# Kernel tuning notes

Hardware: AMD Instinct MI355X
Metric: run time of the kernel (lower is better)

## Reference

```python
import jax, jax.numpy as jnp
import numpy as np

K = 4  # cross2d scan directions


def _selective_scan(u, delta, A, Bs, Cs, Ds, delta_bias):
    # u, delta: (B, K*D, L); A: (K*D, N); Bs, Cs: (B, K, N, L); Ds: (K*D,)
    Bsz, KD, L = u.shape
    D = KD // K
    N = A.shape[1]
    delta = jax.nn.softplus(delta + delta_bias[None, :, None])
    u4 = u.reshape(Bsz, K, D, L)
    dl = delta.reshape(Bsz, K, D, L)
    A4 = A.reshape(K, D, N)

    def step(h, inp):
        dl_t, u_t, B_t, C_t = inp  # (B,K,D),(B,K,D),(B,K,N),(B,K,N)
        dA = jnp.exp(dl_t[..., None] * A4)                     # (B,K,D,N)
        h = dA * h + (dl_t * u_t)[..., None] * B_t[:, :, None, :]
        y = jnp.einsum('bkdn,bkn->bkd', h, C_t)
        return h, y

    h0 = jnp.zeros((Bsz, K, D, N), u.dtype)
    inps = (jnp.moveaxis(dl, -1, 0), jnp.moveaxis(u4, -1, 0),
            jnp.moveaxis(Bs, -1, 0), jnp.moveaxis(Cs, -1, 0))
    _, ys = jax.lax.scan(step, h0, inps)                       # (L,B,K,D)
    ys = jnp.moveaxis(ys, 0, -1)                               # (B,K,D,L)
    return ys + Ds.reshape(1, K, D, 1) * u4


def setup_inputs() -> dict:
    key = jax.random.key(0)
    ks = jax.random.split(key, 12)
    B, H, W, d_model = 8, 48, 48, 96
    d_inner, N, R = 192, 16, 6
    s = 0.05
    return {
        'x': jax.random.normal(ks[0], (B, H, W, d_model), jnp.float32),
        'in_proj_w': jax.random.normal(ks[1], (2 * d_inner, d_model), jnp.float32) * s,
        'conv_w': jax.random.normal(ks[2], (d_inner, 1, 3, 3), jnp.float32) * s,
        'conv_b': jax.random.normal(ks[3], (d_inner,), jnp.float32) * s,
        'x_proj_w': jax.random.normal(ks[4], (K, R + 2 * N, d_inner), jnp.float32) * s,
        'dt_projs_w': jax.random.normal(ks[5], (K, d_inner, R), jnp.float32) * s,
        'dt_projs_b': jax.random.normal(ks[6], (K, d_inner), jnp.float32) * s,
        'A_logs': jax.random.uniform(ks[7], (K * d_inner, N), jnp.float32),
        'Ds': jax.random.normal(ks[8], (K * d_inner,), jnp.float32) * s,
        'ln_g': jnp.ones((d_inner,), jnp.float32),
        'ln_b': jnp.zeros((d_inner,), jnp.float32),
        'out_proj_w': jax.random.normal(ks[9], (d_model, d_inner), jnp.float32) * s,
    }


def reference(x, in_proj_w, conv_w, conv_b, x_proj_w, dt_projs_w, dt_projs_b,
              A_logs, Ds, ln_g, ln_b, out_proj_w):
    B, H, W, _ = x.shape
    Din = dt_projs_w.shape[1]
    N = A_logs.shape[1]
    R = dt_projs_w.shape[2]
    L = H * W

    # in_proj + gate split (channel-last)
    xz = x @ in_proj_w.T                                    # (B,H,W,2*Din)
    xc, z = jnp.split(xz, 2, axis=-1)
    z = jax.nn.silu(z)

    # depthwise conv (NCHW) + SiLU
    xc = jnp.transpose(xc, (0, 3, 1, 2))                    # (B,Din,H,W)
    xc = jax.lax.conv_general_dilated(
        xc, conv_w, (1, 1), 'SAME', feature_group_count=Din,
        dimension_numbers=('NCHW', 'OIHW', 'NCHW')) + conv_b[None, :, None, None]
    xc = jax.nn.silu(xc)

    # cross-scan (cross2d): row-major, col-major, and their reverses
    x0 = xc.reshape(B, Din, L)
    x1 = jnp.transpose(xc, (0, 1, 3, 2)).reshape(B, Din, L)
    xs = jnp.stack([x0, x1, x0[..., ::-1], x1[..., ::-1]], axis=1)  # (B,K,Din,L)

    # grouped projections
    x_dbl = jnp.einsum('bkdl,kcd->bkcl', xs, x_proj_w)
    dts, Bm, Cm = jnp.split(x_dbl, [R, R + N], axis=2)      # (B,K,R,L),(B,K,N,L),(B,K,N,L)
    dts = jnp.einsum('bkrl,kdr->bkdl', dts, dt_projs_w)

    A = -jnp.exp(A_logs.astype(jnp.float32))                # (K*Din, N)
    ys = _selective_scan(xs.reshape(B, K * Din, L), dts.reshape(B, K * Din, L),
                         A, Bm, Cm, Ds.astype(jnp.float32),
                         dt_projs_b.reshape(-1).astype(jnp.float32))  # (B,K,Din,L)

    # cross-merge (inverse of cross-scan)
    y02 = ys[:, 0] + ys[:, 2, :, ::-1]
    y13 = ys[:, 1] + ys[:, 3, :, ::-1]
    y = y02 + jnp.transpose(y13.reshape(B, Din, W, H), (0, 1, 3, 2)).reshape(B, Din, L)
    y = jnp.transpose(y.reshape(B, Din, H, W), (0, 2, 3, 1))  # (B,H,W,Din)

    # LayerNorm over channels
    mu = y.mean(-1, keepdims=True)
    var = y.var(-1, keepdims=True)
    y = (y - mu) / jnp.sqrt(var + 1e-5) * ln_g + ln_b

    y = y * z
    return y @ out_proj_w.T
```

## Files before the change

kernel.cpp:

```cpp
#include <hip/hip_runtime.h>
#include <math.h>

#define HD   48
#define WD   48
#define BB   8
#define DM   96
#define DIN  192
#define LL   2304
#define NN   16
#define RR   6
#define KK   4
#define CH   32
#define NC   72

#define LOG2E 1.44269504f
#define LN2   0.69314718f

__global__ __launch_bounds__(256) void k_inproj(const float* __restrict__ x,
                                                const float* __restrict__ w,
                                                float* __restrict__ xc,
                                                float* __restrict__ zb) {
    __shared__ float sa[64 * 97];
    __shared__ float sb[96 * 68];
    const int tid = threadIdx.x;
    const int p0 = blockIdx.x * 64;
    const int n0 = blockIdx.y * 64;

    for (int i = tid; i < 64 * 96; i += 256) {
        int r = i / 96, c = i % 96;
        sa[r * 97 + c] = x[(size_t)(p0 + r) * 96 + c];
    }
    for (int i = tid; i < 64 * 96; i += 256) {
        int n = i / 96, c = i % 96;
        sb[c * 68 + n] = w[(size_t)(n0 + n) * 96 + c];
    }
    __syncthreads();

    const int tx = tid & 15, ty = tid >> 4;
    const int r0 = ty * 4, c0 = tx * 4;
    float acc[4][4] = {};
    for (int k = 0; k < 96; ++k) {
        float a0 = sa[(r0 + 0) * 97 + k];
        float a1 = sa[(r0 + 1) * 97 + k];
        float a2 = sa[(r0 + 2) * 97 + k];
        float a3 = sa[(r0 + 3) * 97 + k];
        float4 bv = *(const float4*)&sb[k * 68 + c0];
        acc[0][0] += a0 * bv.x; acc[0][1] += a0 * bv.y; acc[0][2] += a0 * bv.z; acc[0][3] += a0 * bv.w;
        acc[1][0] += a1 * bv.x; acc[1][1] += a1 * bv.y; acc[1][2] += a1 * bv.z; acc[1][3] += a1 * bv.w;
        acc[2][0] += a2 * bv.x; acc[2][1] += a2 * bv.y; acc[2][2] += a2 * bv.z; acc[2][3] += a2 * bv.w;
        acc[3][0] += a3 * bv.x; acc[3][1] += a3 * bv.y; acc[3][2] += a3 * bv.z; acc[3][3] += a3 * bv.w;
    }
    for (int i = 0; i < 4; ++i) {
        int p = p0 + r0 + i;
        for (int j = 0; j < 4; ++j) {
            int n = n0 + c0 + j;
            float v = acc[i][j];
            if (n < DIN) {
                xc[(size_t)p * DIN + n] = v;
            } else {
                float s = v / (1.f + __expf(-v));
                zb[(size_t)p * DIN + (n - DIN)] = s;
            }
        }
    }
}

__global__ __launch_bounds__(192) void k_conv(const float* __restrict__ xc,
                                              const float* __restrict__ cw,
                                              const float* __restrict__ cb,
                                              float* __restrict__ xs0,
                                              float* __restrict__ xs1) {
    const int p = blockIdx.x;
    const int d = threadIdx.x;
    const int b = p / LL;
    const int hw = p % LL;
    const int h = hw / WD, w = hw % WD;

    float acc = cb[d];
    #pragma unroll
    for (int ky = 0; ky < 3; ++ky) {
        int hy = h + ky - 1;
        if ((unsigned)hy >= HD) continue;
        #pragma unroll
        for (int kx = 0; kx < 3; ++kx) {
            int wx = w + kx - 1;
            if ((unsigned)wx >= WD) continue;
            acc += xc[((size_t)(b * HD + hy) * WD + wx) * DIN + d] * cw[d * 9 + ky * 3 + kx];
        }
    }
    float v = acc / (1.f + __expf(-acc));
    xs0[((size_t)b * LL + h * WD + w) * DIN + d] = v;
    xs1[((size_t)b * LL + w * HD + h) * DIN + d] = v;
}

__global__ __launch_bounds__(256) void k_xproj(const float* __restrict__ xs0,
                                               const float* __restrict__ xs1,
                                               const float* __restrict__ wxp,
                                               float* __restrict__ dtr,
                                               float* __restrict__ Bt,
                                               float* __restrict__ Ct) {
    __shared__ float sxs[64 * 196];
    __shared__ float sw[40 * 192];
    const int k = blockIdx.y;
    const int b = blockIdx.z;
    const int tid = threadIdx.x;
    const int t0 = blockIdx.x * 64;
    const float* src = (k & 1) ? xs1 : xs0;

    for (int i = tid; i < 40 * 48; i += 256) {
        int row = i / 48, j = i % 48;
        float4 v = (row < 38)
            ? ((const float4*)&wxp[((size_t)k * 38 + row) * 192])[j]
            : make_float4(0.f, 0.f, 0.f, 0.f);
        ((float4*)&sw[row * 192])[j] = v;
    }
    for (int i = tid; i < 64 * 48; i += 256) {
        int r = i / 48, j = i % 48;
        int t = t0 + r;
        int ts = (k < 2) ? t : (LL - 1 - t);
        ((float4*)&sxs[r * 196])[j] =
            ((const float4*)&src[((size_t)b * LL + ts) * DIN])[j];
    }
    __syncthreads();

    const int lp = tid & 31;
    const int c0 = (tid >> 5) * 5;
    float acc[2][5] = {};
    const float* x0 = &sxs[lp * 196];
    const float* x1 = &sxs[(lp + 32) * 196];
    for (int d = 0; d < 192; d += 4) {
        float4 a0 = *(const float4*)&x0[d];
        float4 a1 = *(const float4*)&x1[d];
        #pragma unroll
        for (int j = 0; j < 5; ++j) {
            float4 wv = *(const float4*)&sw[(c0 + j) * 192 + d];
            acc[0][j] += a0.x * wv.x + a0.y * wv.y + a0.z * wv.z + a0.w * wv.w;
            acc[1][j] += a1.x * wv.x + a1.y * wv.y + a1.z * wv.z + a1.w * wv.w;
        }
    }

    #pragma unroll
    for (int pp = 0; pp < 2; ++pp) {
        size_t base = (size_t)(b * KK + k) * LL + (t0 + lp + pp * 32);
        #pragma unroll
        for (int j = 0; j < 5; ++j) {
            int c = c0 + j;
            float v = acc[pp][j];
            if (c < RR)               dtr[base * RR + c] = v;
            else if (c < RR + NN)     Bt[base * NN + (c - RR)] = v;
            else if (c < RR + 2 * NN) Ct[base * NN + (c - RR - NN)] = v;
        }
    }
}

__global__ __launch_bounds__(192) void k_scan1(const float* __restrict__ xs0,
                                               const float* __restrict__ xs1,
                                               const float* __restrict__ dtr,
                                               const float* __restrict__ Bt,
                                               const float* __restrict__ A_logs,
                                               const float* __restrict__ dtw,
                                               const float* __restrict__ dtb,
                                               float* __restrict__ hend,
                                               float* __restrict__ ssp) {
    __shared__ __align__(16) float sB[CH * NN];
    __shared__ __align__(16) float sdt[CH * RR];
    const int c = blockIdx.x, k = blockIdx.y, b = blockIdx.z;
    const int d = threadIdx.x;
    const int kd = k * DIN + d;
    const size_t baseBK = (size_t)(b * KK + k) * LL;
    const int t0 = c * CH;

    for (int i = threadIdx.x; i < CH * NN; i += 192) sB[i] = Bt[(baseBK + t0) * NN + i];
    for (int i = threadIdx.x; i < CH * RR; i += 192) sdt[i] = dtr[(baseBK + t0) * RR + i];
    __syncthreads();

    float a2_[NN];
    #pragma unroll
    for (int n = 0; n < NN; ++n) a2_[n] = -__expf(A_logs[(size_t)kd * NN + n]) * LOG2E;
    float w_[RR];
    #pragma unroll
    for (int r = 0; r < RR; ++r) w_[r] = dtw[(size_t)kd * RR + r];
    const float bias = dtb[kd];
    float h[NN];
    #pragma unroll
    for (int n = 0; n < NN; ++n) h[n] = 0.f;
    float sum_sp = 0.f;

    const float* u_src = (k & 1) ? xs1 : xs0;
    float u_next = u_src[((size_t)b * LL + ((k < 2) ? t0 : (LL - 1 - t0))) * DIN + d];

    for (int tt = 0; tt < CH; ++tt) {
        float u = u_next;
        if (tt + 1 < CH) {
            int tn = t0 + tt + 1;
            int ts = (k < 2) ? tn : (LL - 1 - tn);
            u_next = u_src[((size_t)b * LL + ts) * DIN + d];
        }
        const float2* dr = (const float2*)&sdt[tt * RR];
        float2 d0 = dr[0], d1 = dr[1], d2 = dr[2];
        float xv = bias + d0.x * w_[0] + d0.y * w_[1] + d1.x * w_[2]
                        + d1.y * w_[3] + d2.x * w_[4] + d2.y * w_[5];
        float sp = (xv > 15.f) ? xv
                 : __builtin_amdgcn_logf(1.f + __builtin_amdgcn_exp2f(xv * LOG2E)) * LN2;
        sum_sp += sp;
        float du = sp * u;
        const float4* Bp = (const float4*)&sB[tt * NN];
        #pragma unroll
        for (int q = 0; q < 4; ++q) {
            float4 Bv = Bp[q];
            h[4*q+0] = __builtin_amdgcn_exp2f(sp * a2_[4*q+0]) * h[4*q+0] + du * Bv.x;
            h[4*q+1] = __builtin_amdgcn_exp2f(sp * a2_[4*q+1]) * h[4*q+1] + du * Bv.y;
            h[4*q+2] = __builtin_amdgcn_exp2f(sp * a2_[4*q+2]) * h[4*q+2] + du * Bv.z;
            h[4*q+3] = __builtin_amdgcn_exp2f(sp * a2_[4*q+3]) * h[4*q+3] + du * Bv.w;
        }
    }

    size_t ob = (((size_t)(b * KK + k) * NC + c) * DIN + d) * NN;
    #pragma unroll
    for (int q = 0; q < 4; ++q) {
        *(float4*)&hend[ob + 4 * q] = make_float4(h[4*q], h[4*q+1], h[4*q+2], h[4*q+3]);
    }
    ssp[((size_t)c * (BB * KK) + (b * KK + k)) * DIN + d] = sum_sp;
}

__global__ __launch_bounds__(256) void k_comb(float* __restrict__ hend,
                                              const float* __restrict__ ssp,
                                              const float* __restrict__ A_logs) {
    const int gid = blockIdx.x * 256 + threadIdx.x;
    const int n = gid & 15;
    const int dkb = gid >> 4;
    const int d = dkb % DIN;
    const int bk = dkb / DIN;
    const int k = bk & 3;
    const float a2 = -__expf(A_logs[(size_t)(k * DIN + d) * NN + n]) * LOG2E;
    float h = 0.f;
    for (int c = 0; c < NC; ++c) {
        size_t idx = (((size_t)bk * NC + c) * DIN + d) * NN + n;
        float e = hend[idx];
        hend[idx] = h;
        float P = __builtin_amdgcn_exp2f(a2 * ssp[((size_t)c * (BB * KK) + bk) * DIN + d]);
        h = P * h + e;
    }
}

__global__ __launch_bounds__(192) void k_scan2(const float* __restrict__ xs0,
                                               const float* __restrict__ xs1,
                                               const float* __restrict__ dtr,
                                               const float* __restrict__ Bt,
                                               const float* __restrict__ Ct,
                                               const float* __restrict__ A_logs,
                                               const float* __restrict__ Ds,
                                               const float* __restrict__ dtw,
                                               const float* __restrict__ dtb,
                                               const float* __restrict__ hstart,
                                               float* __restrict__ yacc) {
    __shared__ __align__(16) float sB[CH * NN];
    __shared__ __align__(16) float sC[CH * NN];
    __shared__ __align__(16) float sdt[CH * RR];
    const int c = blockIdx.x, k = blockIdx.y, b = blockIdx.z;
    const int d = threadIdx.x;
    const int kd = k * DIN + d;
    const size_t baseBK = (size_t)(b * KK + k) * LL;
    const int t0 = c * CH;

    for (int i = threadIdx.x; i < CH * NN; i += 192) {
        sB[i] = Bt[(baseBK + t0) * NN + i];
        sC[i] = Ct[(baseBK + t0) * NN + i];
    }
    for (int i = threadIdx.x; i < CH * RR; i += 192) sdt[i] = dtr[(baseBK + t0) * RR + i];
    __syncthreads();

    float a2_[NN];
    #pragma unroll
    for (int n = 0; n < NN; ++n) a2_[n] = -__expf(A_logs[(size_t)kd * NN + n]) * LOG2E;
    float w_[RR];
    #pragma unroll
    for (int r = 0; r < RR; ++r) w_[r] = dtw[(size_t)kd * RR + r];
    const float bias = dtb[kd];
    const float Dv = Ds[kd];

    float h[NN];
    size_t hb = (((size_t)(b * KK + k) * NC + c) * DIN + d) * NN;
    #pragma unroll
    for (int q = 0; q < 4; ++q) {
        float4 hv = *(const float4*)&hstart[hb + 4 * q];
        h[4*q] = hv.x; h[4*q+1] = hv.y; h[4*q+2] = hv.z; h[4*q+3] = hv.w;
    }

    const float* u_src = (k & 1) ? xs1 : xs0;
    float u_next = u_src[((size_t)b * LL + ((k < 2) ? t0 : (LL - 1 - t0))) * DIN + d];

    for (int tt = 0; tt < CH; ++tt) {
        float u = u_next;
        if (tt + 1 < CH) {
            int tn = t0 + tt + 1;
            int ts = (k < 2) ? tn : (LL - 1 - tn);
            u_next = u_src[((size_t)b * LL + ts) * DIN + d];
        }
        const float2* dr = (const float2*)&sdt[tt * RR];
        float2 d0 = dr[0], d1 = dr[1], d2 = dr[2];
        float xv = bias + d0.x * w_[0] + d0.y * w_[1] + d1.x * w_[2]
                        + d1.y * w_[3] + d2.x * w_[4] + d2.y * w_[5];
        float sp = (xv > 15.f) ? xv
                 : __builtin_amdgcn_logf(1.f + __builtin_amdgcn_exp2f(xv * LOG2E)) * LN2;
        float du = sp * u;
        const float4* Bp = (const float4*)&sB[tt * NN];
        const float4* Cp = (const float4*)&sC[tt * NN];
        float y = 0.f;
        #pragma unroll
        for (int q = 0; q < 4; ++q) {
            float4 Bv = Bp[q], Cv = Cp[q];
            h[4*q+0] = __builtin_amdgcn_exp2f(sp * a2_[4*q+0]) * h[4*q+0] + du * Bv.x; y += h[4*q+0] * Cv.x;
            h[4*q+1] = __builtin_amdgcn_exp2f(sp * a2_[4*q+1]) * h[4*q+1] + du * Bv.y; y += h[4*q+1] * Cv.y;
            h[4*q+2] = __builtin_amdgcn_exp2f(sp * a2_[4*q+2]) * h[4*q+2] + du * Bv.z; y += h[4*q+2] * Cv.z;
            h[4*q+3] = __builtin_amdgcn_exp2f(sp * a2_[4*q+3]) * h[4*q+3] + du * Bv.w; y += h[4*q+3] * Cv.w;
        }
        y += Dv * u;

        int t = t0 + tt;
        int pos;
        if (k == 0)      pos = t;
        else if (k == 2) pos = LL - 1 - t;
        else if (k == 1) pos = (t % HD) * WD + (t / HD);
        else { int t1 = LL - 1 - t; pos = (t1 % HD) * WD + (t1 / HD); }

        atomicAdd(&yacc[((size_t)b * LL + pos) * DIN + d], y);
    }
}

__global__ __launch_bounds__(256) void k_final(const float* __restrict__ yacc,
                                               const float* __restrict__ zb,
                                               const float* __restrict__ g,
                                               const float* __restrict__ bta,
                                               const float* __restrict__ wo,
                                               float* __restrict__ out) {
    __shared__ float syn[32 * 194];
    __shared__ float swo[96 * 98];
    const int tid = threadIdx.x;
    const int P0 = blockIdx.x * 32;

    {
        const int p = tid >> 3;
        const int q = tid & 7;
        const float* yr = &yacc[((size_t)(P0 + p)) * DIN + q * 24];
        float4 v0 = ((const float4*)yr)[0];
        float4 v1 = ((const float4*)yr)[1];
        float4 v2 = ((const float4*)yr)[2];
        float4 v3 = ((const float4*)yr)[3];
        float4 v4 = ((const float4*)yr)[4];
        float4 v5 = ((const float4*)yr)[5];
        float s  = v0.x+v0.y+v0.z+v0.w + v1.x+v1.y+v1.z+v1.w + v2.x+v2.y+v2.z+v2.w
                 + v3.x+v3.y+v3.z+v3.w + v4.x+v4.y+v4.z+v4.w + v5.x+v5.y+v5.z+v5.w;
        float sq = v0.x*v0.x+v0.y*v0.y+v0.z*v0.z+v0.w*v0.w
                 + v1.x*v1.x+v1.y*v1.y+v1.z*v1.z+v1.w*v1.w
                 + v2.x*v2.x+v2.y*v2.y+v2.z*v2.z+v2.w*v2.w
                 + v3.x*v3.x+v3.y*v3.y+v3.z*v3.z+v3.w*v3.w
                 + v4.x*v4.x+v4.y*v4.y+v4.z*v4.z+v4.w*v4.w
                 + v5.x*v5.x+v5.y*v5.y+v5.z*v5.z+v5.w*v5.w;
        #pragma unroll
        for (int off = 1; off < 8; off <<= 1) {
            s  += __shfl_xor(s, off);
            sq += __shfl_xor(sq, off);
        }
        float mu = s * (1.f / DIN);
        float rs = rsqrtf(sq * (1.f / DIN) - mu * mu + 1e-5f);

        const float* zr = &zb[((size_t)(P0 + p)) * DIN + q * 24];
        const float* gr = &g[q * 24];
        const float* br = &bta[q * 24];
        float* sy = &syn[p * 194 + q * 24];
        #pragma unroll
        for (int j = 0; j < 6; ++j) {
            float4 vv = (j == 0) ? v0 : (j == 1) ? v1 : (j == 2) ? v2
                      : (j == 3) ? v3 : (j == 4) ? v4 : v5;
            float4 gv = ((const float4*)gr)[j];
            float4 bv = ((const float4*)br)[j];
            float4 zv = ((const float4*)zr)[j];
            float t0 = ((vv.x - mu) * rs * gv.x + bv.x) * zv.x;
            float t1 = ((vv.y - mu) * rs * gv.y + bv.y) * zv.y;
            float t2 = ((vv.z - mu) * rs * gv.z + bv.z) * zv.z;
            float t3 = ((vv.w - mu) * rs * gv.w + bv.w) * zv.w;
            ((float2*)sy)[2 * j]     = make_float2(t0, t1);
            ((float2*)sy)[2 * j + 1] = make_float2(t2, t3);
        }
    }

    const int tx = tid & 15;
    const int ty = tid >> 4;
    const int c0 = tx * 6;
    const int p0 = ty * 2;
    float acc[2][6] = {};

    for (int kb = 0; kb < 2; ++kb) {
        __syncthreads();
        for (int i = tid; i < 96 * 96; i += 256) {
            int n = i / 96, k = i - n * 96;
            swo[k * 98 + n] = wo[(size_t)n * DIN + kb * 96 + k];
        }
        __syncthreads();
        const float* sy0 = &syn[p0 * 194 + kb * 96];
        const float* sy1 = &syn[(p0 + 1) * 194 + kb * 96];
        #pragma unroll 4
        for (int k = 0; k < 96; ++k) {
            float a0 = sy0[k];
            float a1 = sy1[k];
            const float2* wp = (const float2*)&swo[k * 98 + c0];
            float2 w01 = wp[0], w23 = wp[1], w45 = wp[2];
            acc[0][0] += a0 * w01.x; acc[0][1] += a0 * w01.y;
            acc[0][2] += a0 * w23.x; acc[0][3] += a0 * w23.y;
            acc[0][4] += a0 * w45.x; acc[0][5] += a0 * w45.y;
            acc[1][0] += a1 * w01.x; acc[1][1] += a1 * w01.y;
            acc[1][2] += a1 * w23.x; acc[1][3] += a1 * w23.y;
            acc[1][4] += a1 * w45.x; acc[1][5] += a1 * w45.y;
        }
    }

    #pragma unroll
    for (int i = 0; i < 2; ++i) {
        float* orow = &out[((size_t)(P0 + p0 + i)) * DM + c0];
        orow[0] = acc[i][0]; orow[1] = acc[i][1]; orow[2] = acc[i][2];
        orow[3] = acc[i][3]; orow[4] = acc[i][4]; orow[5] = acc[i][5];
    }
}

extern "C" void kernel_launch(void* const* d_in, const int* in_sizes, int n_in,
                              void* d_out, int out_size, void* d_ws, size_t ws_size,
                              hipStream_t stream) {
    const float* x      = (const float*)d_in[0];
    const float* w_in   = (const float*)d_in[1];
    const float* conv_w = (const float*)d_in[2];
    const float* conv_b = (const float*)d_in[3];
    const float* w_xp   = (const float*)d_in[4];
    const float* dtw    = (const float*)d_in[5];
    const float* dtb    = (const float*)d_in[6];
    const float* A_logs = (const float*)d_in[7];
    const float* Ds     = (const float*)d_in[8];
    const float* ln_g   = (const float*)d_in[9];
    const float* ln_b   = (const float*)d_in[10];
    const float* w_out  = (const float*)d_in[11];
    float* out = (float*)d_out;

    float* ws = (float*)d_ws;
    size_t o = 0;
    float* xc  = ws + o; o += (size_t)BB * LL * DIN;
    float* zb  = ws + o; o += (size_t)BB * LL * DIN;
    float* xs0 = ws + o; o += (size_t)BB * LL * DIN;
    float* xs1 = ws + o; o += (size_t)BB * LL * DIN;
    float* Btb = ws + o; o += (size_t)BB * KK * LL * NN;
    float* Ctb = ws + o; o += (size_t)BB * KK * LL * NN;
    float* dtrb= ws + o; o += (size_t)BB * KK * LL * RR;
    float* yac = ws + o; o += (size_t)BB * LL * DIN;
    float* hend= ws + o; o += (size_t)BB * KK * NC * DIN * NN;
    float* ssp = ws + o; o += (size_t)NC * BB * KK * DIN;

    hipMemsetAsync(yac, 0, sizeof(float) * (size_t)BB * LL * DIN, stream);

    dim3 g1(288, 6);
    k_inproj<<<g1, 256, 0, stream>>>(x, w_in, xc, zb);

    k_conv<<<BB * LL, DIN, 0, stream>>>(xc, conv_w, conv_b, xs0, xs1);

    dim3 g3(LL / 64, KK, BB);
    k_xproj<<<g3, 256, 0, stream>>>(xs0, xs1, w_xp, dtrb, Btb, Ctb);

    dim3 gs(NC, KK, BB);
    k_scan1<<<gs, DIN, 0, stream>>>(xs0, xs1, dtrb, Btb, A_logs, dtw, dtb, hend, ssp);
    k_comb<<<(BB * KK * DIN * NN) / 256, 256, 0, stream>>>(hend, ssp, A_logs);
    k_scan2<<<gs, DIN, 0, stream>>>(xs0, xs1, dtrb, Btb, Ctb, A_logs, Ds, dtw, dtb,
                                    hend, yac);

    k_final<<<BB * LL / 32, 256, 0, stream>>>(yac, zb, ln_g, ln_b, w_out, out);
}
```

Baseline: 342.7 us.

## Compute local scan outputs in pass one and add carry-in correction separately

The first chunked scan pass now also computes the chunk-local outputs y (with the D skip term) and stores them per direction. The second pass no longer reruns the recurrence. It adds only the carried-in state contribution C·exp(cumsum(dt)·A)·h0, and skips chunk 0. The cross-merge atomics and the memset are removed; instead the final kernel gathers the four direction outputs with the index permutations before LayerNorm. The cost is a 4x larger ys buffer with extra global writes and reads, plus an extra exp per state in the correction pass.

Measured after the change: 350.3 us. +2.2%, slower.

```diff
diff --git a/kernel.cpp b/kernel.cpp
--- a/kernel.cpp
+++ b/kernel.cpp
@@ -153,16 +153,20 @@
     }
 }
 
-__global__ __launch_bounds__(192) void k_scan1(const float* __restrict__ xs0,
-                                               const float* __restrict__ xs1,
-                                               const float* __restrict__ dtr,
-                                               const float* __restrict__ Bt,
-                                               const float* __restrict__ A_logs,
-                                               const float* __restrict__ dtw,
-                                               const float* __restrict__ dtb,
-                                               float* __restrict__ hend,
-                                               float* __restrict__ ssp) {
+__global__ __launch_bounds__(192) void k_scan(const float* __restrict__ xs0,
+                                              const float* __restrict__ xs1,
+                                              const float* __restrict__ dtr,
+                                              const float* __restrict__ Bt,
+                                              const float* __restrict__ Ct,
+                                              const float* __restrict__ A_logs,
+                                              const float* __restrict__ Ds,
+                                              const float* __restrict__ dtw,
+                                              const float* __restrict__ dtb,
+                                              float* __restrict__ hend,
+                                              float* __restrict__ ssp,
+                                              float* __restrict__ ys) {
     __shared__ __align__(16) float sB[CH * NN];
+    __shared__ __align__(16) float sC[CH * NN];
     __shared__ __align__(16) float sdt[CH * RR];
     const int c = blockIdx.x, k = blockIdx.y, b = blockIdx.z;
     const int d = threadIdx.x;
@@ -170,7 +174,10 @@
     const size_t baseBK = (size_t)(b * KK + k) * LL;
     const int t0 = c * CH;
 
-    for (int i = threadIdx.x; i < CH * NN; i += 192) sB[i] = Bt[(baseBK + t0) * NN + i];
+    for (int i = threadIdx.x; i < CH * NN; i += 192) {
+        sB[i] = Bt[(baseBK + t0) * NN + i];
+        sC[i] = Ct[(baseBK + t0) * NN + i];
+    }
     for (int i = threadIdx.x; i < CH * RR; i += 192) sdt[i] = dtr[(baseBK + t0) * RR + i];
     __syncthreads();
 
@@ -181,6 +188,7 @@
     #pragma unroll
     for (int r = 0; r < RR; ++r) w_[r] = dtw[(size_t)kd * RR + r];
     const float bias = dtb[kd];
+    const float Dv = Ds[kd];
     float h[NN];
     #pragma unroll
     for (int n = 0; n < NN; ++n) h[n] = 0.f;
@@ -205,14 +213,18 @@
         sum_sp += sp;
         float du = sp * u;
         const float4* Bp = (const float4*)&sB[tt * NN];
+        const float4* Cp = (const float4*)&sC[tt * NN];
+        float y = 0.f;
         #pragma unroll
         for (int q = 0; q < 4; ++q) {
-            float4 Bv = Bp[q];
-            h[4*q+0] = __builtin_amdgcn_exp2f(sp * a2_[4*q+0]) * h[4*q+0] + du * Bv.x;
-            h[4*q+1] = __builtin_amdgcn_exp2f(sp * a2_[4*q+1]) * h[4*q+1] + du * Bv.y;
-            h[4*q+2] = __builtin_amdgcn_exp2f(sp * a2_[4*q+2]) * h[4*q+2] + du * Bv.z;
-            h[4*q+3] = __builtin_amdgcn_exp2f(sp * a2_[4*q+3]) * h[4*q+3] + du * Bv.w;
-        }
+            float4 Bv = Bp[q], Cv = Cp[q];
+            h[4*q+0] = __builtin_amdgcn_exp2f(sp * a2_[4*q+0]) * h[4*q+0] + du * Bv.x; y += h[4*q+0] * Cv.x;
+            h[4*q+1] = __builtin_amdgcn_exp2f(sp * a2_[4*q+1]) * h[4*q+1] + du * Bv.y; y += h[4*q+1] * Cv.y;
+            h[4*q+2] = __builtin_amdgcn_exp2f(sp * a2_[4*q+2]) * h[4*q+2] + du * Bv.z; y += h[4*q+2] * Cv.z;
+            h[4*q+3] = __builtin_amdgcn_exp2f(sp * a2_[4*q+3]) * h[4*q+3] + du * Bv.w; y += h[4*q+3] * Cv.w;
+        }
+        y += Dv * u;
+        ys[(baseBK + t0 + tt) * DIN + d] = y;
     }
 
     size_t ob = (((size_t)(b * KK + k) * NC + c) * DIN + d) * NN;
@@ -243,18 +255,14 @@
     }
 }
 
-__global__ __launch_bounds__(192) void k_scan2(const float* __restrict__ xs0,
-                                               const float* __restrict__ xs1,
-                                               const float* __restrict__ dtr,
-                                               const float* __restrict__ Bt,
-                                               const float* __restrict__ Ct,
-                                               const float* __restrict__ A_logs,
-                                               const float* __restrict__ Ds,
-                                               const float* __restrict__ dtw,
-                                               const float* __restrict__ dtb,
-                                               const float* __restrict__ hstart,
-                                               float* __restrict__ yacc) {
-    __shared__ __align__(16) float sB[CH * NN];
+__global__ __launch_bounds__(192) void k_corr(const float* __restrict__ dtr,
+                                              const float* __restrict__ Ct,
+                                              const float* __restrict__ A_logs,
+                                              const float* __restrict__ dtw,
+                                              const float* __restrict__ dtb,
+                                              const float* __restrict__ hstart,
+                                              float* __restrict__ ys) {
+    if (blockIdx.x == 0) return;
     __shared__ __align__(16) float sC[CH * NN];
     __shared__ __align__(16) float sdt[CH * RR];
     const int c = blockIdx.x, k = blockIdx.y, b = blockIdx.z;
@@ -263,10 +271,7 @@
     const size_t baseBK = (size_t)(b * KK + k) * LL;
     const int t0 = c * CH;
 
-    for (int i = threadIdx.x; i < CH * NN; i += 192) {
-        sB[i] = Bt[(baseBK + t0) * NN + i];
-        sC[i] = Ct[(baseBK + t0) * NN + i];
-    }
+    for (int i = threadIdx.x; i < CH * NN; i += 192) sC[i] = Ct[(baseBK + t0) * NN + i];
     for (int i = threadIdx.x; i < CH * RR; i += 192) sdt[i] = dtr[(baseBK + t0) * RR + i];
     __syncthreads();
 
@@ -277,58 +282,40 @@
     #pragma unroll
     for (int r = 0; r < RR; ++r) w_[r] = dtw[(size_t)kd * RR + r];
     const float bias = dtb[kd];
-    const float Dv = Ds[kd];
-
-    float h[NN];
+
+    float h0[NN];
     size_t hb = (((size_t)(b * KK + k) * NC + c) * DIN + d) * NN;
     #pragma unroll
     for (int q = 0; q < 4; ++q) {
         float4 hv = *(const float4*)&hstart[hb + 4 * q];
-        h[4*q] = hv.x; h[4*q+1] = hv.y; h[4*q+2] = hv.z; h[4*q+3] = hv.w;
-    }
-
-    const float* u_src = (k & 1) ? xs1 : xs0;
-    float u_next = u_src[((size_t)b * LL + ((k < 2) ? t0 : (LL - 1 - t0))) * DIN + d];
-
+        h0[4*q] = hv.x; h0[4*q+1] = hv.y; h0[4*q+2] = hv.z; h0[4*q+3] = hv.w;
+    }
+
+    float ssum = 0.f;
     for (int tt = 0; tt < CH; ++tt) {
-        float u = u_next;
-        if (tt + 1 < CH) {
-            int tn = t0 + tt + 1;
-            int ts = (k < 2) ? tn : (LL - 1 - tn);
-            u_next = u_src[((size_t)b * LL + ts) * DIN + d];
-        }
         const float2* dr = (const float2*)&sdt[tt * RR];
         float2 d0 = dr[0], d1 = dr[1], d2 = dr[2];
         float xv = bias + d0.x * w_[0] + d0.y * w_[1] + d1.x * w_[2]
                         + d1.y * w_[3] + d2.x * w_[4] + d2.y * w_[5];
         float sp = (xv > 15.f) ? xv
                  : __builtin_amdgcn_logf(1.f + __builtin_amdgcn_exp2f(xv * LOG2E)) * LN2;
-        float du = sp * u;
-        const float4* Bp = (const float4*)&sB[tt * NN];
+        ssum += sp;
         const float4* Cp = (const float4*)&sC[tt * NN];
-        float y = 0.f;
+        float acc = 0.f;
         #pragma unroll
         for (int q = 0; q < 4; ++q) {
-            float4 Bv = Bp[q], Cv = Cp[q];
-            h[4*q+0] = __builtin_amdgcn_exp2f(sp * a2_[4*q+0]) * h[4*q+0] + du * Bv.x; y += h[4*q+0] * Cv.x;
-            h[4*q+1] = __builtin_amdgcn_exp2f(sp * a2_[4*q+1]) * h[4*q+1] + du * Bv.y; y += h[4*q+1] * Cv.y;
-            h[4*q+2] = __builtin_amdgcn_exp2f(sp * a2_[4*q+2]) * h[4*q+2] + du * Bv.z; y += h[4*q+2] * Cv.z;
-            h[4*q+3] = __builtin_amdgcn_exp2f(sp * a2_[4*q+3]) * h[4*q+3] + du * Bv.w; y += h[4*q+3] * Cv.w;
-        }
-        y += Dv * u;
-
-        int t = t0 + tt;
-        int pos;
-        if (k == 0)      pos = t;
-        else if (k == 2) pos = LL - 1 - t;
-        else if (k == 1) pos = (t % HD) * WD + (t / HD);
-        else { int t1 = LL - 1 - t; pos = (t1 % HD) * WD + (t1 / HD); }
-
-        atomicAdd(&yacc[((size_t)b * LL + pos) * DIN + d], y);
-    }
-}
-
-__global__ __launch_bounds__(256) void k_final(const float* __restrict__ yacc,
+            float4 Cv = Cp[q];
+            acc += Cv.x * (__builtin_amdgcn_exp2f(ssum * a2_[4*q+0]) * h0[4*q+0]);
+            acc += Cv.y * (__builtin_amdgcn_exp2f(ssum * a2_[4*q+1]) * h0[4*q+1]);
+            acc += Cv.z * (__builtin_amdgcn_exp2f(ssum * a2_[4*q+2]) * h0[4*q+2]);
+            acc += Cv.w * (__builtin_amdgcn_exp2f(ssum * a2_[4*q+3]) * h0[4*q+3]);
+        }
+        size_t yi = (baseBK + t0 + tt) * DIN + d;
+        ys[yi] += acc;
+    }
+}
+
+__global__ __launch_bounds__(256) void k_final(const float* __restrict__ ys,
                                                const float* __restrict__ zb,
                                                const float* __restrict__ g,
                                                const float* __restrict__ bta,
@@ -342,21 +329,34 @@
     {
         const int p = tid >> 3;
         const int q = tid & 7;
-        const float* yr = &yacc[((size_t)(P0 + p)) * DIN + q * 24];
-        float4 v0 = ((const float4*)yr)[0];
-        float4 v1 = ((const float4*)yr)[1];
-        float4 v2 = ((const float4*)yr)[2];
-        float4 v3 = ((const float4*)yr)[3];
-        float4 v4 = ((const float4*)yr)[4];
-        float4 v5 = ((const float4*)yr)[5];
-        float s  = v0.x+v0.y+v0.z+v0.w + v1.x+v1.y+v1.z+v1.w + v2.x+v2.y+v2.z+v2.w
-                 + v3.x+v3.y+v3.z+v3.w + v4.x+v4.y+v4.z+v4.w + v5.x+v5.y+v5.z+v5.w;
-        float sq = v0.x*v0.x+v0.y*v0.y+v0.z*v0.z+v0.w*v0.w
-                 + v1.x*v1.x+v1.y*v1.y+v1.z*v1.z+v1.w*v1.w
-                 + v2.x*v2.x+v2.y*v2.y+v2.z*v2.z+v2.w*v2.w
-                 + v3.x*v3.x+v3.y*v3.y+v3.z*v3.z+v3.w*v3.w
-                 + v4.x*v4.x+v4.y*v4.y+v4.z*v4.z+v4.w*v4.w
-                 + v5.x*v5.x+v5.y*v5.y+v5.z*v5.z+v5.w*v5.w;
+        const int P = P0 + p;
+        const int b = P / LL;
+        const int t = P % LL;
+        const int hh = t / WD, ww = t % WD;
+        const int t1 = ww * HD + hh;
+        const float* r0 = &ys[((size_t)(b * KK + 0) * LL + t) * DIN + q * 24];
+        const float* r1 = &ys[((size_t)(b * KK + 1) * LL + t1) * DIN + q * 24];
+        const float* r2 = &ys[((size_t)(b * KK + 2) * LL + (LL - 1 - t)) * DIN + q * 24];
+        const float* r3 = &ys[((size_t)(b * KK + 3) * LL + (LL - 1 - t1)) * DIN + q * 24];
+        float4 va[6];
+        #pragma unroll
+        for (int j = 0; j < 6; ++j) {
+            float4 a = ((const float4*)r0)[j];
+            float4 bb = ((const float4*)r1)[j];
+            float4 cc = ((const float4*)r2)[j];
+            float4 dd = ((const float4*)r3)[j];
+            va[j] = make_float4(a.x + bb.x + cc.x + dd.x,
+                                a.y + bb.y + cc.y + dd.y,
+                                a.z + bb.z + cc.z + dd.z,
+                                a.w + bb.w + cc.w + dd.w);
+        }
+        float s = 0.f, sq = 0.f;
+        #pragma unroll
+        for (int j = 0; j < 6; ++j) {
+            s  += va[j].x + va[j].y + va[j].z + va[j].w;
+            sq += va[j].x * va[j].x + va[j].y * va[j].y
+                + va[j].z * va[j].z + va[j].w * va[j].w;
+        }
         #pragma unroll
         for (int off = 1; off < 8; off <<= 1) {
             s  += __shfl_xor(s, off);
@@ -365,22 +365,20 @@
         float mu = s * (1.f / DIN);
         float rs = rsqrtf(sq * (1.f / DIN) - mu * mu + 1e-5f);
 
-        const float* zr = &zb[((size_t)(P0 + p)) * DIN + q * 24];
+        const float* zr = &zb[((size_t)P) * DIN + q * 24];
         const float* gr = &g[q * 24];
         const float* br = &bta[q * 24];
         float* sy = &syn[p * 194 + q * 24];
         #pragma unroll
         for (int j = 0; j < 6; ++j) {
-            float4 vv = (j == 0) ? v0 : (j == 1) ? v1 : (j == 2) ? v2
-                      : (j == 3) ? v3 : (j == 4) ? v4 : v5;
             float4 gv = ((const float4*)gr)[j];
             float4 bv = ((const float4*)br)[j];
             float4 zv = ((const float4*)zr)[j];
-            float t0 = ((vv.x - mu) * rs * gv.x + bv.x) * zv.x;
-            float t1 = ((vv.y - mu) * rs * gv.y + bv.y) * zv.y;
-            float t2 = ((vv.z - mu) * rs * gv.z + bv.z) * zv.z;
-            float t3 = ((vv.w - mu) * rs * gv.w + bv.w) * zv.w;
-            ((float2*)sy)[2 * j]     = make_float2(t0, t1);
+            float t0 = ((va[j].x - mu) * rs * gv.x + bv.x) * zv.x;
+            float t1_ = ((va[j].y - mu) * rs * gv.y + bv.y) * zv.y;
+            float t2 = ((va[j].z - mu) * rs * gv.z + bv.z) * zv.z;
+            float t3 = ((va[j].w - mu) * rs * gv.w + bv.w) * zv.w;
+            ((float2*)sy)[2 * j]     = make_float2(t0, t1_);
             ((float2*)sy)[2 * j + 1] = make_float2(t2, t3);
         }
     }
@@ -449,12 +447,10 @@
     float* Btb = ws + o; o += (size_t)BB * KK * LL * NN;
     float* Ctb = ws + o; o += (size_t)BB * KK * LL * NN;
     float* dtrb= ws + o; o += (size_t)BB * KK * LL * RR;
-    float* yac = ws + o; o += (size_t)BB * LL * DIN;
+    float* ysb = ws + o; o += (size_t)BB * KK * LL * DIN;
     float* hend= ws + o; o += (size_t)BB * KK * NC * DIN * NN;
     float* ssp = ws + o; o += (size_t)NC * BB * KK * DIN;
 
-    hipMemsetAsync(yac, 0, sizeof(float) * (size_t)BB * LL * DIN, stream);
-
     dim3 g1(288, 6);
     k_inproj<<<g1, 256, 0, stream>>>(x, w_in, xc, zb);
 
@@ -464,10 +460,10 @@
     k_xproj<<<g3, 256, 0, stream>>>(xs0, xs1, w_xp, dtrb, Btb, Ctb);
 
     dim3 gs(NC, KK, BB);
-    k_scan1<<<gs, DIN, 0, stream>>>(xs0, xs1, dtrb, Btb, A_logs, dtw, dtb, hend, ssp);
+    k_scan<<<gs, DIN, 0, stream>>>(xs0, xs1, dtrb, Btb, Ctb, A_logs, Ds, dtw, dtb,
+                                   hend, ssp, ysb);
     k_comb<<<(BB * KK * DIN * NN) / 256, 256, 0, stream>>>(hend, ssp, A_logs);
-    k_scan2<<<gs, DIN, 0, stream>>>(xs0, xs1, dtrb, Btb, Ctb, A_logs, Ds, dtw, dtb,
-                                    hend, yac);
-
-    k_final<<<BB * LL / 32, 256, 0, stream>>>(yac, zb, ln_g, ln_b, w_out, out);
-}
+    k_corr<<<gs, DIN, 0, stream>>>(dtrb, Ctb, A_logs, dtw, dtb, hend, ysb);
+
+    k_final<<<BB * LL / 32, 256, 0, stream>>>(ysb, zb, ln_g, ln_b, w_out, out);
+}
```

## Emit zero-start outputs in first scan pass and add cheap carry-correction pass

Applied to the files above, without the earlier changes.

The first chunked scan pass now computes outputs y from a zero initial state and atomically accumulates them, and the second pass becomes a correction that adds only the carried-in state's contribution, C·exp(A·cumsum(dt))·h0. This removes the full second recurrence, including its B and u loads, and chunk 0 is skipped. The x-projection also reads xs0 once per position and loops over all four directions, scattering results to the permuted direction indices. The cost is extra atomics in the correction pass and a cumulative-softplus exponent that may lose some precision compared with step-by-step products.

After: 366.5 us. +7.0%, slower.

```diff
diff --git a/kernel.cpp b/kernel.cpp
--- a/kernel.cpp
+++ b/kernel.cpp
@@ -94,58 +94,60 @@
 }
 
 __global__ __launch_bounds__(256) void k_xproj(const float* __restrict__ xs0,
-                                               const float* __restrict__ xs1,
                                                const float* __restrict__ wxp,
                                                float* __restrict__ dtr,
                                                float* __restrict__ Bt,
                                                float* __restrict__ Ct) {
-    __shared__ float sxs[64 * 196];
+    __shared__ float sxs[32 * 196];
     __shared__ float sw[40 * 192];
-    const int k = blockIdx.y;
-    const int b = blockIdx.z;
+    const int b = blockIdx.y;
     const int tid = threadIdx.x;
-    const int t0 = blockIdx.x * 64;
-    const float* src = (k & 1) ? xs1 : xs0;
-
-    for (int i = tid; i < 40 * 48; i += 256) {
-        int row = i / 48, j = i % 48;
-        float4 v = (row < 38)
-            ? ((const float4*)&wxp[((size_t)k * 38 + row) * 192])[j]
-            : make_float4(0.f, 0.f, 0.f, 0.f);
-        ((float4*)&sw[row * 192])[j] = v;
-    }
-    for (int i = tid; i < 64 * 48; i += 256) {
+    const int t0 = blockIdx.x * 32;
+
+    for (int i = tid; i < 32 * 48; i += 256) {
         int r = i / 48, j = i % 48;
-        int t = t0 + r;
-        int ts = (k < 2) ? t : (LL - 1 - t);
         ((float4*)&sxs[r * 196])[j] =
-            ((const float4*)&src[((size_t)b * LL + ts) * DIN])[j];
-    }
-    __syncthreads();
+            ((const float4*)&xs0[((size_t)b * LL + t0 + r) * DIN])[j];
+    }
 
     const int lp = tid & 31;
     const int c0 = (tid >> 5) * 5;
-    float acc[2][5] = {};
-    const float* x0 = &sxs[lp * 196];
-    const float* x1 = &sxs[(lp + 32) * 196];
-    for (int d = 0; d < 192; d += 4) {
-        float4 a0 = *(const float4*)&x0[d];
-        float4 a1 = *(const float4*)&x1[d];
-        #pragma unroll
-        for (int j = 0; j < 5; ++j) {
-            float4 wv = *(const float4*)&sw[(c0 + j) * 192 + d];
-            acc[0][j] += a0.x * wv.x + a0.y * wv.y + a0.z * wv.z + a0.w * wv.w;
-            acc[1][j] += a1.x * wv.x + a1.y * wv.y + a1.z * wv.z + a1.w * wv.w;
-        }
-    }
-
-    #pragma unroll
-    for (int pp = 0; pp < 2; ++pp) {
-        size_t base = (size_t)(b * KK + k) * LL + (t0 + lp + pp * 32);
+    const int t = t0 + lp;
+    const int hh = t / WD, ww = t % WD;
+    const int t1 = ww * HD + hh;
+
+    for (int k = 0; k < KK; ++k) {
+        __syncthreads();
+        for (int i = tid; i < 40 * 48; i += 256) {
+            int row = i / 48, j = i % 48;
+            float4 v = (row < 38)
+                ? ((const float4*)&wxp[((size_t)k * 38 + row) * 192])[j]
+                : make_float4(0.f, 0.f, 0.f, 0.f);
+            ((float4*)&sw[row * 192])[j] = v;
+        }
+        __syncthreads();
+
+        float acc[5] = {};
+        const float* x0 = &sxs[lp * 196];
+        for (int d = 0; d < 192; d += 4) {
+            float4 a0 = *(const float4*)&x0[d];
+            #pragma unroll
+            for (int j = 0; j < 5; ++j) {
+                float4 wv = *(const float4*)&sw[(c0 + j) * 192 + d];
+                acc[j] += a0.x * wv.x + a0.y * wv.y + a0.z * wv.z + a0.w * wv.w;
+            }
+        }
+
+        int tk;
+        if (k == 0)      tk = t;
+        else if (k == 1) tk = t1;
+        else if (k == 2) tk = LL - 1 - t;
+        else             tk = LL - 1 - t1;
+        size_t base = (size_t)(b * KK + k) * LL + tk;
         #pragma unroll
         for (int j = 0; j < 5; ++j) {
             int c = c0 + j;
-            float v = acc[pp][j];
+            float v = acc[j];
             if (c < RR)               dtr[base * RR + c] = v;
             else if (c < RR + NN)     Bt[base * NN + (c - RR)] = v;
             else if (c < RR + 2 * NN) Ct[base * NN + (c - RR - NN)] = v;
@@ -153,16 +155,20 @@
     }
 }
 
-__global__ __launch_bounds__(192) void k_scan1(const float* __restrict__ xs0,
-                                               const float* __restrict__ xs1,
-                                               const float* __restrict__ dtr,
-                                               const float* __restrict__ Bt,
-                                               const float* __restrict__ A_logs,
-                                               const float* __restrict__ dtw,
-                                               const float* __restrict__ dtb,
-                                               float* __restrict__ hend,
-                                               float* __restrict__ ssp) {
+__global__ __launch_bounds__(192) void k_scan(const float* __restrict__ xs0,
+                                              const float* __restrict__ xs1,
+                                              const float* __restrict__ dtr,
+                                              const float* __restrict__ Bt,
+                                              const float* __restrict__ Ct,
+                                              const float* __restrict__ A_logs,
+                                              const float* __restrict__ Ds,
+                                              const float* __restrict__ dtw,
+                                              const float* __restrict__ dtb,
+                                              float* __restrict__ hend,
+                                              float* __restrict__ ssp,
+                                              float* __restrict__ yacc) {
     __shared__ __align__(16) float sB[CH * NN];
+    __shared__ __align__(16) float sC[CH * NN];
     __shared__ __align__(16) float sdt[CH * RR];
     const int c = blockIdx.x, k = blockIdx.y, b = blockIdx.z;
     const int d = threadIdx.x;
@@ -170,7 +176,10 @@
     const size_t baseBK = (size_t)(b * KK + k) * LL;
     const int t0 = c * CH;
 
-    for (int i = threadIdx.x; i < CH * NN; i += 192) sB[i] = Bt[(baseBK + t0) * NN + i];
+    for (int i = threadIdx.x; i < CH * NN; i += 192) {
+        sB[i] = Bt[(baseBK + t0) * NN + i];
+        sC[i] = Ct[(baseBK + t0) * NN + i];
+    }
     for (int i = threadIdx.x; i < CH * RR; i += 192) sdt[i] = dtr[(baseBK + t0) * RR + i];
     __syncthreads();
 
@@ -181,6 +190,7 @@
     #pragma unroll
     for (int r = 0; r < RR; ++r) w_[r] = dtw[(size_t)kd * RR + r];
     const float bias = dtb[kd];
+    const float Dv = Ds[kd];
     float h[NN];
     #pragma unroll
     for (int n = 0; n < NN; ++n) h[n] = 0.f;
@@ -205,14 +215,26 @@
         sum_sp += sp;
         float du = sp * u;
         const float4* Bp = (const float4*)&sB[tt * NN];
+        const float4* Cp = (const float4*)&sC[tt * NN];
+        float y = 0.f;
         #pragma unroll
         for (int q = 0; q < 4; ++q) {
-            float4 Bv = Bp[q];
-            h[4*q+0] = __builtin_amdgcn_exp2f(sp * a2_[4*q+0]) * h[4*q+0] + du * Bv.x;
-            h[4*q+1] = __builtin_amdgcn_exp2f(sp * a2_[4*q+1]) * h[4*q+1] + du * Bv.y;
-            h[4*q+2] = __builtin_amdgcn_exp2f(sp * a2_[4*q+2]) * h[4*q+2] + du * Bv.z;
-            h[4*q+3] = __builtin_amdgcn_exp2f(sp * a2_[4*q+3]) * h[4*q+3] + du * Bv.w;
-        }
+            float4 Bv = Bp[q], Cv = Cp[q];
+            h[4*q+0] = __builtin_amdgcn_exp2f(sp * a2_[4*q+0]) * h[4*q+0] + du * Bv.x; y += h[4*q+0] * Cv.x;
+            h[4*q+1] = __builtin_amdgcn_exp2f(sp * a2_[4*q+1]) * h[4*q+1] + du * Bv.y; y += h[4*q+1] * Cv.y;
+            h[4*q+2] = __builtin_amdgcn_exp2f(sp * a2_[4*q+2]) * h[4*q+2] + du * Bv.z; y += h[4*q+2] * Cv.z;
+            h[4*q+3] = __builtin_amdgcn_exp2f(sp * a2_[4*q+3]) * h[4*q+3] + du * Bv.w; y += h[4*q+3] * Cv.w;
+        }
+        y += Dv * u;
+
+        int t = t0 + tt;
+        int pos;
+        if (k == 0)      pos = t;
+        else if (k == 2) pos = LL - 1 - t;
+        else if (k == 1) pos = (t % HD) * WD + (t / HD);
+        else { int tr = LL - 1 - t; pos = (tr % HD) * WD + (tr / HD); }
+
+        atomicAdd(&yacc[((size_t)b * LL + pos) * DIN + d], y);
     }
 
     size_t ob = (((size_t)(b * KK + k) * NC + c) * DIN + d) * NN;
@@ -243,18 +265,14 @@
     }
 }
 
-__global__ __launch_bounds__(192) void k_scan2(const float* __restrict__ xs0,
-                                               const float* __restrict__ xs1,
-                                               const float* __restrict__ dtr,
-                                               const float* __restrict__ Bt,
-                                               const float* __restrict__ Ct,
-                                               const float* __restrict__ A_logs,
-                                               const float* __restrict__ Ds,
-                                               const float* __restrict__ dtw,
-                                               const float* __restrict__ dtb,
-                                               const float* __restrict__ hstart,
-                                               float* __restrict__ yacc) {
-    __shared__ __align__(16) float sB[CH * NN];
+__global__ __launch_bounds__(192) void k_corr(const float* __restrict__ dtr,
+                                              const float* __restrict__ Ct,
+                                              const float* __restrict__ A_logs,
+                                              const float* __restrict__ dtw,
+                                              const float* __restrict__ dtb,
+                                              const float* __restrict__ hstart,
+                                              float* __restrict__ yacc) {
+    if (blockIdx.x == 0) return;
     __shared__ __align__(16) float sC[CH * NN];
     __shared__ __align__(16) float sdt[CH * RR];
     const int c = blockIdx.x, k = blockIdx.y, b = blockIdx.z;
@@ -263,10 +281,7 @@
     const size_t baseBK = (size_t)(b * KK + k) * LL;
     const int t0 = c * CH;
 
-    for (int i = threadIdx.x; i < CH * NN; i += 192) {
-        sB[i] = Bt[(baseBK + t0) * NN + i];
-        sC[i] = Ct[(baseBK + t0) * NN + i];
-    }
+    for (int i = threadIdx.x; i < CH * NN; i += 192) sC[i] = Ct[(baseBK + t0) * NN + i];
     for (int i = threadIdx.x; i < CH * RR; i += 192) sdt[i] = dtr[(baseBK + t0) * RR + i];
     __syncthreads();
 
@@ -277,54 +292,43 @@
     #pragma unroll
     for (int r = 0; r < RR; ++r) w_[r] = dtw[(size_t)kd * RR + r];
     const float bias = dtb[kd];
-    const float Dv = Ds[kd];
-
-    float h[NN];
+
+    float h0[NN];
     size_t hb = (((size_t)(b * KK + k) * NC + c) * DIN + d) * NN;
     #pragma unroll
     for (int q = 0; q < 4; ++q) {
         float4 hv = *(const float4*)&hstart[hb + 4 * q];
-        h[4*q] = hv.x; h[4*q+1] = hv.y; h[4*q+2] = hv.z; h[4*q+3] = hv.w;
-    }
-
-    const float* u_src = (k & 1) ? xs1 : xs0;
-    float u_next = u_src[((size_t)b * LL + ((k < 2) ? t0 : (LL - 1 - t0))) * DIN + d];
-
+        h0[4*q] = hv.x; h0[4*q+1] = hv.y; h0[4*q+2] = hv.z; h0[4*q+3] = hv.w;
+    }
+
+    float ssum = 0.f;
     for (int tt = 0; tt < CH; ++tt) {
-        float u = u_next;
-        if (tt + 1 < CH) {
-            int tn = t0 + tt + 1;
-            int ts = (k < 2) ? tn : (LL - 1 - tn);
-            u_next = u_src[((size_t)b * LL + ts) * DIN + d];
-        }
         const float2* dr = (const float2*)&sdt[tt * RR];
         float2 d0 = dr[0], d1 = dr[1], d2 = dr[2];
         float xv = bias + d0.x * w_[0] + d0.y * w_[1] + d1.x * w_[2]
                         + d1.y * w_[3] + d2.x * w_[4] + d2.y * w_[5];
         float sp = (xv > 15.f) ? xv
                  : __builtin_amdgcn_logf(1.f + __builtin_amdgcn_exp2f(xv * LOG2E)) * LN2;
-        float du = sp * u;
-        const float4* Bp = (const float4*)&sB[tt * NN];
+        ssum += sp;
         const float4* Cp = (const float4*)&sC[tt * NN];
-        float y = 0.f;
+        float acc = 0.f;
         #pragma unroll
         for (int q = 0; q < 4; ++q) {
-            float4 Bv = Bp[q], Cv = Cp[q];
-            h[4*q+0] = __builtin_amdgcn_exp2f(sp * a2_[4*q+0]) * h[4*q+0] + du * Bv.x; y += h[4*q+0] * Cv.x;
-            h[4*q+1] = __builtin_amdgcn_exp2f(sp * a2_[4*q+1]) * h[4*q+1] + du * Bv.y; y += h[4*q+1] * Cv.y;
-            h[4*q+2] = __builtin_amdgcn_exp2f(sp * a2_[4*q+2]) * h[4*q+2] + du * Bv.z; y += h[4*q+2] * Cv.z;
-            h[4*q+3] = __builtin_amdgcn_exp2f(sp * a2_[4*q+3]) * h[4*q+3] + du * Bv.w; y += h[4*q+3] * Cv.w;
-        }
-        y += Dv * u;
+            float4 Cv = Cp[q];
+            acc += Cv.x * (__builtin_amdgcn_exp2f(ssum * a2_[4*q+0]) * h0[4*q+0]);
+            acc += Cv.y * (__builtin_amdgcn_exp2f(ssum * a2_[4*q+1]) * h0[4*q+1]);
+            acc += Cv.z * (__builtin_amdgcn_exp2f(ssum * a2_[4*q+2]) * h0[4*q+2]);
+            acc += Cv.w * (__builtin_amdgcn_exp2f(ssum * a2_[4*q+3]) * h0[4*q+3]);
+        }
 
         int t = t0 + tt;
         int pos;
         if (k == 0)      pos = t;
         else if (k == 2) pos = LL - 1 - t;
         else if (k == 1) pos = (t % HD) * WD + (t / HD);
-        else { int t1 = LL - 1 - t; pos = (t1 % HD) * WD + (t1 / HD); }
-
-        atomicAdd(&yacc[((size_t)b * LL + pos) * DIN + d], y);
+        else { int tr = LL - 1 - t; pos = (tr % HD) * WD + (tr / HD); }
+
+        atomicAdd(&yacc[((size_t)b * LL + pos) * DIN + d], acc);
     }
 }
 
@@ -460,14 +464,14 @@
 
     k_conv<<<BB * LL, DIN, 0, stream>>>(xc, conv_w, conv_b, xs0, xs1);
 
-    dim3 g3(LL / 64, KK, BB);
-    k_xproj<<<g3, 256, 0, stream>>>(xs0, xs1, w_xp, dtrb, Btb, Ctb);
+    dim3 g3(LL / 32, BB);
+    k_xproj<<<g3, 256, 0, stream>>>(xs0, w_xp, dtrb, Btb, Ctb);
 
     dim3 gs(NC, KK, BB);
-    k_scan1<<<gs, DIN, 0, stream>>>(xs0, xs1, dtrb, Btb, A_logs, dtw, dtb, hend, ssp);
+    k_scan<<<gs, DIN, 0, stream>>>(xs0, xs1, dtrb, Btb, Ctb, A_logs, Ds, dtw, dtb,
+                                   hend, ssp, yac);
     k_comb<<<(BB * KK * DIN * NN) / 256, 256, 0, stream>>>(hend, ssp, A_logs);
-    k_scan2<<<gs, DIN, 0, stream>>>(xs0, xs1, dtrb, Btb, Ctb, A_logs, Ds, dtw, dtb,
-                                    hend, yac);
+    k_corr<<<gs, DIN, 0, stream>>>(dtrb, Ctb, A_logs, dtw, dtb, hend, yac);
 
     k_final<<<BB * LL / 32, 256, 0, stream>>>(yac, zb, ln_g, ln_b, w_out, out);
 }
```
